# Kernel optimization log

Measured on AMD Instinct MI355X. Metric: run time of the kernel, lower is better.

## Reference

```python
import jax, jax.numpy as jnp
import numpy as np

D_MODEL = 1024
NUM_HEADS = 16
D_K = D_MODEL // NUM_HEADS
B, T = 2, 2048


def setup_inputs() -> dict:
    key = jax.random.key(0)
    ks = jax.random.split(key, 11)
    s = 1.0 / np.sqrt(D_MODEL)
    inp = {
        "q": jax.random.normal(ks[0], (B, T, D_MODEL), jnp.float32),
        "k": jax.random.normal(ks[1], (B, T, D_MODEL), jnp.float32),
        "v": jax.random.normal(ks[2], (B, T, D_MODEL), jnp.float32),
        "mask": jnp.tril(jnp.ones((1, 1, T, T), jnp.int32)),  # causal
        "wq": jax.random.normal(ks[3], (D_MODEL, D_MODEL), jnp.float32) * s,
        "bq": jnp.zeros((D_MODEL,), jnp.float32),
        "wk": jax.random.normal(ks[4], (D_MODEL, D_MODEL), jnp.float32) * s,
        "bk": jnp.zeros((D_MODEL,), jnp.float32),
        "wv": jax.random.normal(ks[5], (D_MODEL, D_MODEL), jnp.float32) * s,
        "bv": jnp.zeros((D_MODEL,), jnp.float32),
        "wo": jax.random.normal(ks[6], (D_MODEL, D_MODEL), jnp.float32) * s,
        "bo": jnp.zeros((D_MODEL,), jnp.float32),
    }
    return inp


def reference(q, k, v, mask, wq, bq, wk, bk, wv, bv, wo, bo):
    Bq, Tq, _ = q.shape
    Tk = k.shape[1]
    # projections, split into heads: (B, H, T, d_k)
    qh = (q @ wq + bq).reshape(Bq, Tq, NUM_HEADS, D_K).transpose(0, 2, 1, 3)
    kh = (k @ wk + bk).reshape(Bq, Tk, NUM_HEADS, D_K).transpose(0, 2, 1, 3)
    vh = (v @ wv + bv).reshape(Bq, Tk, NUM_HEADS, D_K).transpose(0, 2, 1, 3)
    scores = jnp.einsum("bhqd,bhkd->bhqk", qh, kh) / jnp.sqrt(jnp.float32(D_K))
    scores = jnp.where(mask == 0, jnp.float32(-1e9), scores)
    attn = jax.nn.softmax(scores, axis=-1)
    ctx = jnp.einsum("bhqk,bhkd->bhqd", attn, vh)
    ctx = ctx.transpose(0, 2, 1, 3).reshape(Bq, Tq, D_MODEL)
    return ctx @ wo + bo
```

## Files before the change

### kernel.cpp

```cpp
#include <hip/hip_runtime.h>
#include <hip/hip_bf16.h>

#define DM 1024
#define NH 16
#define DK 64
#define TT 2048
#define BATCH 2

typedef __attribute__((ext_vector_type(8))) short bf16x8;
typedef __attribute__((ext_vector_type(4))) float f32x4;
typedef __attribute__((ext_vector_type(4))) unsigned short u16x4;
typedef unsigned short u16;

__device__ inline u16 f2b(float x){ __hip_bfloat16 h = __float2bfloat16(x); return *reinterpret_cast<u16*>(&h); }

__device__ inline void gl_lds16(const u16* g, u16* l) {
  __builtin_amdgcn_global_load_lds(
      (const __attribute__((address_space(1))) unsigned int*)g,
      (__attribute__((address_space(3))) unsigned int*)l, 16, 0, 0);
}

__global__ __launch_bounds__(256) void prep(const float* __restrict__ q, const float* __restrict__ k,
                                            const float* __restrict__ v,
                                            const float* __restrict__ wq, const float* __restrict__ wk,
                                            const float* __restrict__ wv, const float* __restrict__ wo,
                                            u16* __restrict__ qb, u16* __restrict__ kb,
                                            u16* __restrict__ vb, u16* __restrict__ wt) {
  int z = blockIdx.z;
  if (z < 3) {
    const float* src = z==0 ? q : z==1 ? k : v;
    u16* dst = z==0 ? qb : z==1 ? kb : vb;
    size_t i = ((size_t)blockIdx.x*256 + threadIdx.x)*8;
    f32x4 a = *(const f32x4*)(src+i);
    f32x4 b = *(const f32x4*)(src+i+4);
    union { bf16x8 v8; u16 e[8]; } u;
    #pragma unroll
    for (int j=0;j<4;j++){ u.e[j] = f2b(a[j]); u.e[4+j] = f2b(b[j]); }
    *(bf16x8*)(dst+i) = u.v8;
  } else {
    int bx = blockIdx.x;
    if (bx >= 1024) return;
    __shared__ float tile[32][33];
    const float* src = z==3 ? wq : z==4 ? wk : z==5 ? wv : wo;
    u16* dst = wt + (size_t)(z-3)*DM*DM;
    int bxx = bx & 31, byy = bx >> 5;
    int tx = threadIdx.x & 31, ty = threadIdx.x >> 5;
    int x  = bxx*32 + tx;
    int y0 = byy*32 + ty;
    #pragma unroll
    for (int i=0;i<32;i+=8) tile[ty+i][tx] = src[(size_t)(y0+i)*DM + x];
    __syncthreads();
    int xo = byy*32 + tx;
    int yo = bxx*32 + ty;
    #pragma unroll
    for (int i=0;i<32;i+=8) dst[(size_t)(yo+i)*DM + xo] = f2b(tile[tx][ty+i]);
  }
}

__global__ __launch_bounds__(256) void gemm_qkv(const u16* __restrict__ qb, const u16* __restrict__ kb,
                                                const u16* __restrict__ vb, const u16* __restrict__ wt,
                                                const float* __restrict__ bq, const float* __restrict__ bk,
                                                const float* __restrict__ bv,
                                                u16* __restrict__ qh, u16* __restrict__ kh,
                                                u16* __restrict__ vhT) {
  const int z = blockIdx.z;
  const u16* A = z==0 ? qb : z==1 ? kb : vb;
  const u16* W = wt + (size_t)z*DM*DM;
  const float* bias = z==0 ? bq : z==1 ? bk : bv;
  u16* outv = z==0 ? qh : z==1 ? kh : vhT;
  const int mode = (z==2) ? 1 : 0;
  const float oscale = (z==0) ? 0.125f : 1.0f;

  __shared__ u16 As[2][128*32];
  __shared__ u16 Bs[2][128*32];
  const int tid = threadIdx.x, lane = tid & 63, wid = tid >> 6;
  const int li = lane & 15, quad = lane >> 4;
  const int row0 = blockIdx.x*128, col0 = blockIdx.y*128;
  const int wr = wid & 1, wc = wid >> 1;

  f32x4 acc[4][4];
  #pragma unroll
  for (int i=0;i<4;i++)
    #pragma unroll
    for (int j=0;j<4;j++) acc[i][j] = f32x4{0.f,0.f,0.f,0.f};

  const int srow = lane >> 2;
  const int scol = (lane & 3) * 8;

  for (int k0 = 0; k0 < DM; k0 += 64) {
    __syncthreads();
    #pragma unroll
    for (int s=0;s<2;s++)
      #pragma unroll
      for (int c=0;c<2;c++) {
        int ch = wid*2 + c;
        gl_lds16(A + (size_t)(row0 + ch*16 + srow)*DM + k0 + s*32 + scol, As[s] + ch*512);
        gl_lds16(W + (size_t)(col0 + ch*16 + srow)*DM + k0 + s*32 + scol, Bs[s] + ch*512);
      }
    __syncthreads();
    #pragma unroll
    for (int s=0;s<2;s++) {
      bf16x8 a[4], b[4];
      #pragma unroll
      for (int i=0;i<4;i++) a[i] = *(const bf16x8*)&As[s][(wr*64 + i*16 + li)*32 + quad*8];
      #pragma unroll
      for (int j=0;j<4;j++) b[j] = *(const bf16x8*)&Bs[s][(wc*64 + j*16 + li)*32 + quad*8];
      #pragma unroll
      for (int i=0;i<4;i++)
        #pragma unroll
        for (int j=0;j<4;j++)
          acc[i][j] = __builtin_amdgcn_mfma_f32_16x16x32_bf16(a[i], b[j], acc[i][j], 0,0,0);
    }
  }

  #pragma unroll
  for (int j=0;j<4;j++) {
    int col = col0 + wc*64 + j*16 + li;
    float bsv = bias[col];
    #pragma unroll
    for (int i=0;i<4;i++) {
      #pragma unroll
      for (int r=0;r<4;r++) {
        int row = row0 + wr*64 + i*16 + quad*4 + r;
        float vv = (acc[i][j][r] + bsv) * oscale;
        int bb = row >> 11, t = row & (TT-1);
        int hh = col >> 6,  d = col & 63;
        size_t idx = (mode == 0)
          ? ((((size_t)(bb*NH + hh)*TT + t) << 6) + d)
          : ((((size_t)(bb*NH + hh)*DK + d)*TT) + t);
        outv[idx] = f2b(vv);
      }
    }
  }
}

__global__ __launch_bounds__(256) void gemm_out64(const u16* __restrict__ A, const u16* __restrict__ W,
                                                  const float* __restrict__ bias, float* __restrict__ out) {
  __shared__ u16 As[2][128*32];
  __shared__ u16 Bs[2][64*32];
  const int tid = threadIdx.x, lane = tid & 63, wid = tid >> 6;
  const int li = lane & 15, quad = lane >> 4;
  const int row0 = blockIdx.x*128, col0 = blockIdx.y*64;
  const int wr = wid & 1, wc = wid >> 1;

  f32x4 acc[4][2];
  #pragma unroll
  for (int i=0;i<4;i++)
    #pragma unroll
    for (int j=0;j<2;j++) acc[i][j] = f32x4{0.f,0.f,0.f,0.f};

  const int srow = lane >> 2;
  const int scol = (lane & 3) * 8;

  for (int k0 = 0; k0 < DM; k0 += 64) {
    __syncthreads();
    #pragma unroll
    for (int s=0;s<2;s++) {
      #pragma unroll
      for (int c=0;c<2;c++) {
        int ch = wid*2 + c;
        gl_lds16(A + (size_t)(row0 + ch*16 + srow)*DM + k0 + s*32 + scol, As[s] + ch*512);
      }
      gl_lds16(W + (size_t)(col0 + wid*16 + srow)*DM + k0 + s*32 + scol, Bs[s] + wid*512);
    }
    __syncthreads();
    #pragma unroll
    for (int s=0;s<2;s++) {
      bf16x8 a[4], b[2];
      #pragma unroll
      for (int i=0;i<4;i++) a[i] = *(const bf16x8*)&As[s][(wr*64 + i*16 + li)*32 + quad*8];
      #pragma unroll
      for (int j=0;j<2;j++) b[j] = *(const bf16x8*)&Bs[s][(wc*32 + j*16 + li)*32 + quad*8];
      #pragma unroll
      for (int i=0;i<4;i++)
        #pragma unroll
        for (int j=0;j<2;j++)
          acc[i][j] = __builtin_amdgcn_mfma_f32_16x16x32_bf16(a[i], b[j], acc[i][j], 0,0,0);
    }
  }

  #pragma unroll
  for (int j=0;j<2;j++) {
    int col = col0 + wc*32 + j*16 + li;
    float bsv = bias[col];
    #pragma unroll
    for (int i=0;i<4;i++) {
      #pragma unroll
      for (int r=0;r<4;r++) {
        int row = row0 + wr*64 + i*16 + quad*4 + r;
        out[(size_t)row*DM + col] = acc[i][j][r] + bsv;
      }
    }
  }
}

__global__ __launch_bounds__(256) void flash(const u16* __restrict__ qh, const u16* __restrict__ kh,
                                             const u16* __restrict__ vhT, u16* __restrict__ ctx) {
  const int bh = blockIdx.x;
  const int pr = blockIdx.y;
  const int b = bh >> 4, h = bh & 15;
  const u16* Q  = qh  + (size_t)bh*TT*DK;
  const u16* K  = kh  + (size_t)bh*TT*DK;
  const u16* Vt = vhT + (size_t)bh*DK*TT;

  const int tid = threadIdx.x, lane = tid & 63, wid = tid >> 6;
  const int li = lane & 15, quad = lane >> 4;

  __shared__ u16 Kl[64][72];
  __shared__ u16 Vl[64][72];
  __shared__ u16 Pb[4][16][72];

  const int sr = tid >> 3;
  const int sc = (tid & 7) * 8;

  bf16x8 kr0 = *(const bf16x8*)&K[(size_t)(sr   )*DK + sc];
  bf16x8 kr1 = *(const bf16x8*)&K[(size_t)(sr+32)*DK + sc];
  bf16x8 vr0 = *(const bf16x8*)&Vt[(size_t)(sr   )*TT + sc];
  bf16x8 vr1 = *(const bf16x8*)&Vt[(size_t)(sr+32)*TT + sc];

  #pragma unroll
  for (int ph = 0; ph < 2; ph++) {
    const int qt = (ph == 0) ? pr : (31 - pr);
    const int nt = qt + 1;
    const int qrow0 = qt*64 + wid*16;

    bf16x8 qf0 = *(const bf16x8*)&Q[(size_t)(qrow0+li)*DK +      quad*8];
    bf16x8 qf1 = *(const bf16x8*)&Q[(size_t)(qrow0+li)*DK + 32 + quad*8];

    f32x4 o[4];
    #pragma unroll
    for (int d=0;d<4;d++) o[d] = f32x4{0.f,0.f,0.f,0.f};
    float lp = 0.f;

    for (int it = 0; it < nt; it++) {
      const int k0 = it*64;
      __syncthreads();
      *(bf16x8*)&Kl[sr   ][sc] = kr0;
      *(bf16x8*)&Kl[sr+32][sc] = kr1;
      *(bf16x8*)&Vl[sr   ][sc] = vr0;
      *(bf16x8*)&Vl[sr+32][sc] = vr1;
      __syncthreads();
      if (it+1 < nt) {
        const int k1 = k0 + 64;
        kr0 = *(const bf16x8*)&K[(size_t)(k1+sr   )*DK + sc];
        kr1 = *(const bf16x8*)&K[(size_t)(k1+sr+32)*DK + sc];
        vr0 = *(const bf16x8*)&Vt[(size_t)(sr   )*TT + k1 + sc];
        vr1 = *(const bf16x8*)&Vt[(size_t)(sr+32)*TT + k1 + sc];
      } else if (ph == 0) {
        kr0 = *(const bf16x8*)&K[(size_t)(sr   )*DK + sc];
        kr1 = *(const bf16x8*)&K[(size_t)(sr+32)*DK + sc];
        vr0 = *(const bf16x8*)&Vt[(size_t)(sr   )*TT + sc];
        vr1 = *(const bf16x8*)&Vt[(size_t)(sr+32)*TT + sc];
      }

      f32x4 s[4];
      #pragma unroll
      for (int c=0;c<4;c++) {
        bf16x8 kf0 = *(const bf16x8*)&Kl[c*16+li][     quad*8];
        bf16x8 kf1 = *(const bf16x8*)&Kl[c*16+li][32 + quad*8];
        f32x4 t = __builtin_amdgcn_mfma_f32_16x16x32_bf16(kf0, qf0, f32x4{0.f,0.f,0.f,0.f}, 0,0,0);
        s[c]    = __builtin_amdgcn_mfma_f32_16x16x32_bf16(kf1, qf1, t, 0,0,0);
      }
      const bool dg = (it == nt-1);
      const int qq = qrow0 + li;
      float p[4][4];
      if (dg) {
        #pragma unroll
        for (int c=0;c<4;c++)
          #pragma unroll
          for (int r=0;r<4;r++){
            int key = k0 + c*16 + quad*4 + r;
            p[c][r] = (key <= qq) ? __expf(s[c][r]) : 0.f;
          }
      } else {
        #pragma unroll
        for (int c=0;c<4;c++)
          #pragma unroll
          for (int r=0;r<4;r++)
            p[c][r] = __expf(s[c][r]);
      }
      #pragma unroll
      for (int c=0;c<4;c++)
        #pragma unroll
        for (int r=0;r<4;r++)
          lp += p[c][r];

      #pragma unroll
      for (int c=0;c<4;c++) {
        u16x4 w;
        #pragma unroll
        for (int r=0;r<4;r++) w[r] = f2b(p[c][r]);
        *(u16x4*)&Pb[wid][li][c*16 + quad*4] = w;
      }
      __builtin_amdgcn_wave_barrier();
      __asm__ __volatile__("s_waitcnt lgkmcnt(0)");
      bf16x8 pf0 = *(const bf16x8*)&Pb[wid][li][     quad*8];
      bf16x8 pf1 = *(const bf16x8*)&Pb[wid][li][32 + quad*8];

      #pragma unroll
      for (int d=0;d<4;d++){
        bf16x8 vf0 = *(const bf16x8*)&Vl[d*16+li][     quad*8];
        bf16x8 vf1 = *(const bf16x8*)&Vl[d*16+li][32 + quad*8];
        o[d] = __builtin_amdgcn_mfma_f32_16x16x32_bf16(vf0, pf0, o[d], 0,0,0);
        o[d] = __builtin_amdgcn_mfma_f32_16x16x32_bf16(vf1, pf1, o[d], 0,0,0);
      }
    }

    lp += __shfl_xor(lp, 16, 64);
    lp += __shfl_xor(lp, 32, 64);
    float rl = 1.0f / lp;

    const int qq = qrow0 + li;
    #pragma unroll
    for (int d=0;d<4;d++){
      u16x4 w;
      #pragma unroll
      for (int r=0;r<4;r++) w[r] = f2b(o[d][r] * rl);
      *(u16x4*)&ctx[(size_t)(b*TT + qq)*DM + h*DK + d*16 + quad*4] = w;
    }
  }
}

extern "C" void kernel_launch(void* const* d_in, const int* in_sizes, int n_in,
                              void* d_out, int out_size, void* d_ws, size_t ws_size,
                              hipStream_t stream) {
  const float* q   = (const float*)d_in[0];
  const float* k   = (const float*)d_in[1];
  const float* v   = (const float*)d_in[2];
  const float* wq  = (const float*)d_in[4];
  const float* bq  = (const float*)d_in[5];
  const float* wk  = (const float*)d_in[6];
  const float* bk  = (const float*)d_in[7];
  const float* wv  = (const float*)d_in[8];
  const float* bv  = (const float*)d_in[9];
  const float* wo  = (const float*)d_in[10];
  const float* bo  = (const float*)d_in[11];
  float* out = (float*)d_out;

  const size_t SZ = (size_t)BATCH*TT*DM;
  u16* wt  = (u16*)d_ws;
  u16* qb  = wt + (size_t)4*DM*DM;
  u16* kb  = qb + SZ;
  u16* vb  = kb + SZ;
  u16* qh  = vb + SZ;
  u16* kh  = qh + SZ;
  u16* vhT = kh + SZ;
  u16* ctx = qb;

  prep<<<dim3(2048, 1, 7), 256, 0, stream>>>(q, k, v, wq, wk, wv, wo, qb, kb, vb, wt);

  gemm_qkv<<<dim3(4096/128, DM/128, 3), 256, 0, stream>>>(qb, kb, vb, wt, bq, bk, bv, qh, kh, vhT);

  flash<<<dim3(BATCH*NH, 16), 256, 0, stream>>>(qh, kh, vhT, ctx);

  gemm_out64<<<dim3(4096/128, DM/64), 256, 0, stream>>>(ctx, wt + (size_t)3*DM*DM, bo, out);
}
```

Baseline: 237.8 us.

## Triple-buffer GEMM LDS pipeline with swizzle, and write Q/K row-major

Both GEMM kernels move from a two-barrier double-stage loop to a three-buffer pipeline. Loads run two k-steps ahead, with explicit vmcnt waits and a single barrier per step, and MFMA is raised to higher priority. LDS rows get an XOR swizzle to cut bank conflicts. The QKV epilogue now writes Q/K in plain row-major (B,T,DM) layout and packs V^T stores into 4-wide vectors, and the flash kernel reads Q/K with a DM stride to match. The cost is more LDS per block, and correctness depends on the hand-written waitcnt counts.

```diff
diff --git a/kernel.cpp b/kernel.cpp
--- a/kernel.cpp
+++ b/kernel.cpp
@@ -71,64 +71,89 @@
   const int mode = (z==2) ? 1 : 0;
   const float oscale = (z==0) ? 0.125f : 1.0f;
 
-  __shared__ u16 As[2][128*32];
-  __shared__ u16 Bs[2][128*32];
+  __shared__ __align__(16) u16 As[3][128*32];
+  __shared__ __align__(16) u16 Bs[3][128*32];
   const int tid = threadIdx.x, lane = tid & 63, wid = tid >> 6;
   const int li = lane & 15, quad = lane >> 4;
   const int row0 = blockIdx.x*128, col0 = blockIdx.y*128;
   const int wr = wid & 1, wc = wid >> 1;
 
+  const int srow = lane >> 2;
+  const int scol = ((lane & 3) ^ ((srow >> 1) & 3)) * 8;
+  const int rsw  = (li >> 1) & 3;
+
+  auto stage = [&](int hh, int bufi) {
+    const int kk = hh*32;
+    #pragma unroll
+    for (int c=0;c<2;c++) {
+      int ch = wid*2 + c;
+      gl_lds16(A + (size_t)(row0 + ch*16 + srow)*DM + kk + scol, &As[bufi][ch*512]);
+      gl_lds16(W + (size_t)(col0 + ch*16 + srow)*DM + kk + scol, &Bs[bufi][ch*512]);
+    }
+  };
+
   f32x4 acc[4][4];
   #pragma unroll
   for (int i=0;i<4;i++)
     #pragma unroll
     for (int j=0;j<4;j++) acc[i][j] = f32x4{0.f,0.f,0.f,0.f};
 
-  const int srow = lane >> 2;
-  const int scol = (lane & 3) * 8;
-
-  for (int k0 = 0; k0 < DM; k0 += 64) {
-    __syncthreads();
-    #pragma unroll
-    for (int s=0;s<2;s++)
-      #pragma unroll
-      for (int c=0;c<2;c++) {
-        int ch = wid*2 + c;
-        gl_lds16(A + (size_t)(row0 + ch*16 + srow)*DM + k0 + s*32 + scol, As[s] + ch*512);
-        gl_lds16(W + (size_t)(col0 + ch*16 + srow)*DM + k0 + s*32 + scol, Bs[s] + ch*512);
-      }
-    __syncthreads();
-    #pragma unroll
-    for (int s=0;s<2;s++) {
-      bf16x8 a[4], b[4];
-      #pragma unroll
-      for (int i=0;i<4;i++) a[i] = *(const bf16x8*)&As[s][(wr*64 + i*16 + li)*32 + quad*8];
-      #pragma unroll
-      for (int j=0;j<4;j++) b[j] = *(const bf16x8*)&Bs[s][(wc*64 + j*16 + li)*32 + quad*8];
-      #pragma unroll
-      for (int i=0;i<4;i++)
-        #pragma unroll
-        for (int j=0;j<4;j++)
-          acc[i][j] = __builtin_amdgcn_mfma_f32_16x16x32_bf16(a[i], b[j], acc[i][j], 0,0,0);
-    }
-  }
-
-  #pragma unroll
-  for (int j=0;j<4;j++) {
-    int col = col0 + wc*64 + j*16 + li;
-    float bsv = bias[col];
-    #pragma unroll
-    for (int i=0;i<4;i++) {
-      #pragma unroll
-      for (int r=0;r<4;r++) {
-        int row = row0 + wr*64 + i*16 + quad*4 + r;
-        float vv = (acc[i][j][r] + bsv) * oscale;
-        int bb = row >> 11, t = row & (TT-1);
-        int hh = col >> 6,  d = col & 63;
-        size_t idx = (mode == 0)
-          ? ((((size_t)(bb*NH + hh)*TT + t) << 6) + d)
-          : ((((size_t)(bb*NH + hh)*DK + d)*TT) + t);
-        outv[idx] = f2b(vv);
+  stage(0, 0);
+  stage(1, 1);
+  asm volatile("s_waitcnt vmcnt(4)" ::: "memory");
+  __builtin_amdgcn_s_barrier();
+
+  int buf = 0;
+  for (int h = 0; h < 32; h++) {
+    bf16x8 a[4], b[4];
+    #pragma unroll
+    for (int i=0;i<4;i++) a[i] = *(const bf16x8*)&As[buf][(wr*64 + i*16 + li)*32 + (quad ^ rsw)*8];
+    #pragma unroll
+    for (int j=0;j<4;j++) b[j] = *(const bf16x8*)&Bs[buf][(wc*64 + j*16 + li)*32 + (quad ^ rsw)*8];
+
+    if (h < 30) { int nb = buf + 2; if (nb >= 3) nb -= 3; stage(h+2, nb); }
+
+    __builtin_amdgcn_s_setprio(1);
+    #pragma unroll
+    for (int i=0;i<4;i++)
+      #pragma unroll
+      for (int j=0;j<4;j++)
+        acc[i][j] = __builtin_amdgcn_mfma_f32_16x16x32_bf16(a[i], b[j], acc[i][j], 0,0,0);
+    __builtin_amdgcn_s_setprio(0);
+
+    if (h < 30)       asm volatile("s_waitcnt vmcnt(4)" ::: "memory");
+    else if (h == 30) asm volatile("s_waitcnt vmcnt(0)" ::: "memory");
+    __builtin_amdgcn_s_barrier();
+    if (++buf == 3) buf = 0;
+  }
+
+  if (mode == 0) {
+    #pragma unroll
+    for (int j=0;j<4;j++) {
+      int col = col0 + wc*64 + j*16 + li;
+      float bsv = bias[col];
+      #pragma unroll
+      for (int i=0;i<4;i++) {
+        int rowb = row0 + wr*64 + i*16 + quad*4;
+        #pragma unroll
+        for (int r=0;r<4;r++)
+          outv[(size_t)(rowb + r)*DM + col] = f2b((acc[i][j][r] + bsv) * oscale);
+      }
+    }
+  } else {
+    #pragma unroll
+    for (int j=0;j<4;j++) {
+      int col = col0 + wc*64 + j*16 + li;
+      float bsv = bias[col];
+      int hh = col >> 6, d = col & 63;
+      #pragma unroll
+      for (int i=0;i<4;i++) {
+        int rowb = row0 + wr*64 + i*16 + quad*4;
+        int bb = rowb >> 11, t0 = rowb & (TT-1);
+        u16x4 w;
+        #pragma unroll
+        for (int r=0;r<4;r++) w[r] = f2b(acc[i][j][r] + bsv);
+        *(u16x4*)&outv[(((size_t)(bb*NH + hh)*DK + d)*TT) + t0] = w;
       }
     }
   }
@@ -136,47 +161,60 @@
 
 __global__ __launch_bounds__(256) void gemm_out64(const u16* __restrict__ A, const u16* __restrict__ W,
                                                   const float* __restrict__ bias, float* __restrict__ out) {
-  __shared__ u16 As[2][128*32];
-  __shared__ u16 Bs[2][64*32];
+  __shared__ __align__(16) u16 As[3][128*32];
+  __shared__ __align__(16) u16 Bs[3][64*32];
   const int tid = threadIdx.x, lane = tid & 63, wid = tid >> 6;
   const int li = lane & 15, quad = lane >> 4;
   const int row0 = blockIdx.x*128, col0 = blockIdx.y*64;
   const int wr = wid & 1, wc = wid >> 1;
 
+  const int srow = lane >> 2;
+  const int scol = ((lane & 3) ^ ((srow >> 1) & 3)) * 8;
+  const int rsw  = (li >> 1) & 3;
+
+  auto stage = [&](int hh, int bufi) {
+    const int kk = hh*32;
+    #pragma unroll
+    for (int c=0;c<2;c++) {
+      int ch = wid*2 + c;
+      gl_lds16(A + (size_t)(row0 + ch*16 + srow)*DM + kk + scol, &As[bufi][ch*512]);
+    }
+    gl_lds16(W + (size_t)(col0 + wid*16 + srow)*DM + kk + scol, &Bs[bufi][wid*512]);
+  };
+
   f32x4 acc[4][2];
   #pragma unroll
   for (int i=0;i<4;i++)
     #pragma unroll
     for (int j=0;j<2;j++) acc[i][j] = f32x4{0.f,0.f,0.f,0.f};
 
-  const int srow = lane >> 2;
-  const int scol = (lane & 3) * 8;
-
-  for (int k0 = 0; k0 < DM; k0 += 64) {
-    __syncthreads();
-    #pragma unroll
-    for (int s=0;s<2;s++) {
-      #pragma unroll
-      for (int c=0;c<2;c++) {
-        int ch = wid*2 + c;
-        gl_lds16(A + (size_t)(row0 + ch*16 + srow)*DM + k0 + s*32 + scol, As[s] + ch*512);
-      }
-      gl_lds16(W + (size_t)(col0 + wid*16 + srow)*DM + k0 + s*32 + scol, Bs[s] + wid*512);
-    }
-    __syncthreads();
-    #pragma unroll
-    for (int s=0;s<2;s++) {
-      bf16x8 a[4], b[2];
-      #pragma unroll
-      for (int i=0;i<4;i++) a[i] = *(const bf16x8*)&As[s][(wr*64 + i*16 + li)*32 + quad*8];
-      #pragma unroll
-      for (int j=0;j<2;j++) b[j] = *(const bf16x8*)&Bs[s][(wc*32 + j*16 + li)*32 + quad*8];
-      #pragma unroll
-      for (int i=0;i<4;i++)
-        #pragma unroll
-        for (int j=0;j<2;j++)
-          acc[i][j] = __builtin_amdgcn_mfma_f32_16x16x32_bf16(a[i], b[j], acc[i][j], 0,0,0);
-    }
+  stage(0, 0);
+  stage(1, 1);
+  asm volatile("s_waitcnt vmcnt(3)" ::: "memory");
+  __builtin_amdgcn_s_barrier();
+
+  int buf = 0;
+  for (int h = 0; h < 32; h++) {
+    bf16x8 a[4], b[2];
+    #pragma unroll
+    for (int i=0;i<4;i++) a[i] = *(const bf16x8*)&As[buf][(wr*64 + i*16 + li)*32 + (quad ^ rsw)*8];
+    #pragma unroll
+    for (int j=0;j<2;j++) b[j] = *(const bf16x8*)&Bs[buf][(wc*32 + j*16 + li)*32 + (quad ^ rsw)*8];
+
+    if (h < 30) { int nb = buf + 2; if (nb >= 3) nb -= 3; stage(h+2, nb); }
+
+    __builtin_amdgcn_s_setprio(1);
+    #pragma unroll
+    for (int i=0;i<4;i++)
+      #pragma unroll
+      for (int j=0;j<2;j++)
+        acc[i][j] = __builtin_amdgcn_mfma_f32_16x16x32_bf16(a[i], b[j], acc[i][j], 0,0,0);
+    __builtin_amdgcn_s_setprio(0);
+
+    if (h < 30)       asm volatile("s_waitcnt vmcnt(3)" ::: "memory");
+    else if (h == 30) asm volatile("s_waitcnt vmcnt(0)" ::: "memory");
+    __builtin_amdgcn_s_barrier();
+    if (++buf == 3) buf = 0;
   }
 
   #pragma unroll
@@ -199,8 +237,8 @@
   const int bh = blockIdx.x;
   const int pr = blockIdx.y;
   const int b = bh >> 4, h = bh & 15;
-  const u16* Q  = qh  + (size_t)bh*TT*DK;
-  const u16* K  = kh  + (size_t)bh*TT*DK;
+  const u16* Q  = qh  + (size_t)b*TT*DM + h*DK;
+  const u16* K  = kh  + (size_t)b*TT*DM + h*DK;
   const u16* Vt = vhT + (size_t)bh*DK*TT;
 
   const int tid = threadIdx.x, lane = tid & 63, wid = tid >> 6;
@@ -213,8 +251,8 @@
   const int sr = tid >> 3;
   const int sc = (tid & 7) * 8;
 
-  bf16x8 kr0 = *(const bf16x8*)&K[(size_t)(sr   )*DK + sc];
-  bf16x8 kr1 = *(const bf16x8*)&K[(size_t)(sr+32)*DK + sc];
+  bf16x8 kr0 = *(const bf16x8*)&K[(size_t)(sr   )*DM + sc];
+  bf16x8 kr1 = *(const bf16x8*)&K[(size_t)(sr+32)*DM + sc];
   bf16x8 vr0 = *(const bf16x8*)&Vt[(size_t)(sr   )*TT + sc];
   bf16x8 vr1 = *(const bf16x8*)&Vt[(size_t)(sr+32)*TT + sc];
 
@@ -224,8 +262,8 @@
     const int nt = qt + 1;
     const int qrow0 = qt*64 + wid*16;
 
-    bf16x8 qf0 = *(const bf16x8*)&Q[(size_t)(qrow0+li)*DK +      quad*8];
-    bf16x8 qf1 = *(const bf16x8*)&Q[(size_t)(qrow0+li)*DK + 32 + quad*8];
+    bf16x8 qf0 = *(const bf16x8*)&Q[(size_t)(qrow0+li)*DM +      quad*8];
+    bf16x8 qf1 = *(const bf16x8*)&Q[(size_t)(qrow0+li)*DM + 32 + quad*8];
 
     f32x4 o[4];
     #pragma unroll
@@ -242,13 +280,13 @@
       __syncthreads();
       if (it+1 < nt) {
         const int k1 = k0 + 64;
-        kr0 = *(const bf16x8*)&K[(size_t)(k1+sr   )*DK + sc];
-        kr1 = *(const bf16x8*)&K[(size_t)(k1+sr+32)*DK + sc];
+        kr0 = *(const bf16x8*)&K[(size_t)(k1+sr   )*DM + sc];
+        kr1 = *(const bf16x8*)&K[(size_t)(k1+sr+32)*DM + sc];
         vr0 = *(const bf16x8*)&Vt[(size_t)(sr   )*TT + k1 + sc];
         vr1 = *(const bf16x8*)&Vt[(size_t)(sr+32)*TT + k1 + sc];
       } else if (ph == 0) {
-        kr0 = *(const bf16x8*)&K[(size_t)(sr   )*DK + sc];
-        kr1 = *(const bf16x8*)&K[(size_t)(sr+32)*DK + sc];
+        kr0 = *(const bf16x8*)&K[(size_t)(sr   )*DM + sc];
+        kr1 = *(const bf16x8*)&K[(size_t)(sr+32)*DM + sc];
         vr0 = *(const bf16x8*)&Vt[(size_t)(sr   )*TT + sc];
         vr1 = *(const bf16x8*)&Vt[(size_t)(sr+32)*TT + sc];
       }
```

After: 224.6 us. 1.06x faster.
